# Performance work log

Measured on AMD Instinct MI355X. Metric: run time of the kernel, lower is better.

## Reference

```python
import jax, jax.numpy as jnp
from jax import lax
import numpy as np


def setup_inputs() -> dict:
    key = jax.random.key(0)
    k1, k2, k3 = jax.random.split(key, 3)
    B, H, W, C = 8, 128, 128, 128
    F, KS = 128, 3
    x = jax.random.normal(k1, (B, H, W, C), dtype=jnp.float32)
    style = jax.random.normal(k2, (B, C), dtype=jnp.float32)
    kernel = jax.random.normal(k3, (KS, KS, C, F), dtype=jnp.float32) * 0.05
    return {"x": x, "style": style, "kernel": kernel}


def reference(x, style, kernel):
    """StyleGAN2 modulated+demodulated conv via grouped conv (groups=batch).
    x: (B,H,W,C) NHWC, style: (B,C), kernel: (kh,kw,C,F)."""
    B, H, W, C = x.shape
    kh, kw, Cin, F = kernel.shape
    # Modulate: per-sample scale of input channels -> (B, kh, kw, C, F)
    w = kernel[None] * (style[:, None, None, :, None] + 1.0)
    # Demodulate: normalize each output filter over (kh, kw, Cin)
    w = w / jnp.sqrt(jnp.sum(jnp.square(w), axis=(1, 2, 3), keepdims=True) + 1e-8)
    # Grouped conv trick: fold batch into channels, groups = B
    xg = jnp.transpose(x, (0, 3, 1, 2)).reshape(1, B * C, H, W)   # (1, B*C, H, W)
    wg = jnp.transpose(w, (1, 2, 3, 0, 4)).reshape(kh, kw, Cin, B * F)  # HWIO
    y = lax.conv_general_dilated(
        xg, wg, window_strides=(1, 1), padding="SAME",
        dimension_numbers=("NCHW", "HWIO", "NCHW"),
        feature_group_count=B,
    )  # (1, B*F, H, W)
    y = y.reshape(B, F, H, W)
    return jnp.transpose(y, (0, 2, 3, 1))  # NHWC
```

## Files before the change

kernel.cpp:

```cpp
#include <hip/hip_runtime.h>

typedef __attribute__((ext_vector_type(8))) short short8;
typedef __attribute__((ext_vector_type(8))) unsigned short ushort8;
typedef __attribute__((ext_vector_type(4))) float f32x4;

static __device__ __forceinline__ unsigned short f2bf(float f) {
    union { float f; unsigned int u; } a; a.f = f;
    unsigned int u = a.u;
    return (unsigned short)((u + 0x7fffu + ((u >> 16) & 1u)) >> 16);
}

static __device__ __forceinline__ void gll16(const unsigned short* g, unsigned short* l) {
    __builtin_amdgcn_global_load_lds(
        (const __attribute__((address_space(1))) unsigned int*)g,
        (__attribute__((address_space(3))) unsigned int*)l, 16, 0, 0);
}

__global__ void prep_sumsq(const float* __restrict__ kern,
                           const float* __restrict__ style,
                           float* __restrict__ partial) {
    const int rs = blockIdx.x;
    const int b  = blockIdx.y;
    const int t  = threadIdx.x;
    __shared__ float sty[128];
    __shared__ float red[256];
    if (t < 128) sty[t] = style[b * 128 + t] + 1.0f;
    __syncthreads();
    const int f = t & 127, half = t >> 7;
    const float* kp = kern + (size_t)rs * 16384 + f;
    float s = 0.0f;
    #pragma unroll 8
    for (int c = half * 64; c < half * 64 + 64; ++c) {
        float w = kp[(size_t)c * 128] * sty[c];
        s += w * w;
    }
    red[t] = s;
    __syncthreads();
    if (t < 128) partial[((size_t)b * 9 + rs) * 128 + t] = red[t] + red[t + 128];
}

__global__ void prep_wt(const float* __restrict__ kern,
                        const float* __restrict__ style,
                        const float* __restrict__ partial,
                        unsigned short* __restrict__ wt) {
    const int rs = blockIdx.x, b = blockIdx.y;
    const int t  = threadIdx.x;
    __shared__ float sty[128], dm[128];
    __shared__ float ts[32][132];
    if (t < 128) {
        sty[t] = style[b * 128 + t] + 1.0f;
    } else {
        const int f = t - 128;
        float s = 0.0f;
        #pragma unroll
        for (int r = 0; r < 9; ++r) s += partial[((size_t)b * 9 + r) * 128 + f];
        dm[f] = rsqrtf(s + 1e-8f);
    }
    __syncthreads();
    const float* kp = kern + (size_t)rs * 16384;
    unsigned short* wp = wt + ((size_t)b * 9 + rs) * 16384;
    for (int c0 = 0; c0 < 128; c0 += 32) {
        {
            const int fi = (t & 31) * 4;
            const int ci = t >> 5;
            #pragma unroll
            for (int k = 0; k < 4; ++k) {
                const float4 v = *(const float4*)(kp + (size_t)(c0 + ci + 8 * k) * 128 + fi);
                ts[ci + 8 * k][fi + 0] = v.x;
                ts[ci + 8 * k][fi + 1] = v.y;
                ts[ci + 8 * k][fi + 2] = v.z;
                ts[ci + 8 * k][fi + 3] = v.w;
            }
        }
        __syncthreads();
        {
            const int cb = (t & 7) * 4;
            const int f2 = t >> 3;
            #pragma unroll
            for (int k = 0; k < 4; ++k) {
                const int f = f2 + 32 * k;
                ushort4 o;
                o.x = f2bf(ts[cb + 0][f] * sty[c0 + cb + 0] * dm[f]);
                o.y = f2bf(ts[cb + 1][f] * sty[c0 + cb + 1] * dm[f]);
                o.z = f2bf(ts[cb + 2][f] * sty[c0 + cb + 2] * dm[f]);
                o.w = f2bf(ts[cb + 3][f] * sty[c0 + cb + 3] * dm[f]);
                *(ushort4*)(wp + (size_t)f * 128 + c0 + cb) = o;
            }
        }
        __syncthreads();
    }
}

#define PROW 16640
#define PPLANE 2163200
__global__ void cvt_x(const float* __restrict__ x, unsigned short* __restrict__ xbf) {
    const int id = blockIdx.x * 256 + threadIdx.x;
    if (id >= 8 * 130 * 130 * 16) return;
    const int cg = id & 15;
    const int p  = id >> 4;
    const int wp = p % 130;
    const int q  = p / 130;
    const int hp = q % 130;
    const int b  = q / 130;
    ushort8 v = {0, 0, 0, 0, 0, 0, 0, 0};
    if (hp >= 1 && hp <= 128 && wp >= 1 && wp <= 128) {
        const float4* src = (const float4*)(x + (((size_t)b * 128 + (hp - 1)) * 128 + (wp - 1)) * 128 + cg * 8);
        float4 f0 = src[0];
        float4 f1 = src[1];
        v[0] = f2bf(f0.x); v[1] = f2bf(f0.y); v[2] = f2bf(f0.z); v[3] = f2bf(f0.w);
        v[4] = f2bf(f1.x); v[5] = f2bf(f1.y); v[6] = f2bf(f1.z); v[7] = f2bf(f1.w);
    }
    *(ushort8*)(xbf + (size_t)p * 128 + cg * 8) = v;
}

__global__ __launch_bounds__(256, 4) void mdconv6(const unsigned short* __restrict__ xbf,
                                                  const unsigned short* __restrict__ wt,
                                                  float* __restrict__ out) {
    const int lin = blockIdx.x;
    const int b   = lin & 7;
    const int h   = lin >> 3;
    const int tid = threadIdx.x;

    __shared__ unsigned short lsh[2 * 8192];

    const unsigned short* xb  = xbf + (size_t)b * PPLANE;
    const unsigned short* wtb = wt + (size_t)b * 9 * 16384;

    const int a0off = (tid >> 2) * 128 + (tid & 3) * 8;

    const int lane = tid & 63;
    const int wv   = tid >> 6;
    const int fl   = lane & 15;
    const int quad = lane >> 4;
    const int wrb  = (wv >> 1) * 64;
    const int fcb  = (wv & 1) * 64;
    const int ab_rd = (wrb + fl) * 32 + quad * 8;
    const int bb_rd = 4096 + (fcb + fl) * 32 + quad * 8;

    f32x4 acc[4][4];
    #pragma unroll
    for (int mt = 0; mt < 4; ++mt)
        #pragma unroll
        for (int ft = 0; ft < 4; ++ft)
            acc[mt][ft] = (f32x4){0.f, 0.f, 0.f, 0.f};

#define STAGE(st, nxt) {                                                          \
    const int rs_ = (st) >> 2, kc_ = (st) & 3;                                    \
    const int r_ = rs_ / 3, s_ = rs_ % 3;                                         \
    const unsigned short* ga = xb + ((size_t)(h + r_) * 130 + s_) * 128 + kc_ * 32; \
    const unsigned short* gb = wtb + rs_ * 16384 + kc_ * 32;                      \
    unsigned short* la = lsh + (nxt) * 8192;                                      \
    gll16(ga + a0off,        la + tid * 8);                                       \
    gll16(ga + a0off + 8192, la + 2048 + tid * 8);                                \
    gll16(gb + a0off,        la + 4096 + tid * 8);                                \
    gll16(gb + a0off + 8192, la + 6144 + tid * 8);                                \
}

    STAGE(0, 0);
    __syncthreads();

    #pragma unroll
    for (int st = 0; st < 36; ++st) {
        const int cur = st & 1;
        if (st < 35) STAGE(st + 1, cur ^ 1);
        const int ce = cur * 8192;
        short8 bv[4];
        #pragma unroll
        for (int ft = 0; ft < 4; ++ft)
            bv[ft] = *(const short8*)(lsh + ce + bb_rd + ft * 512);
        #pragma unroll
        for (int mt = 0; mt < 4; ++mt) {
            const short8 av = *(const short8*)(lsh + ce + ab_rd + mt * 512);
            #pragma unroll
            for (int ft = 0; ft < 4; ++ft)
                acc[mt][ft] = __builtin_amdgcn_mfma_f32_16x16x32_bf16(av, bv[ft], acc[mt][ft], 0, 0, 0);
        }
        __syncthreads();
    }
#undef STAGE

    float* ob = out + ((size_t)(b * 128 + h) * 128) * 128;
    #pragma unroll
    for (int mt = 0; mt < 4; ++mt) {
        #pragma unroll
        for (int reg = 0; reg < 4; ++reg) {
            const int w = wrb + mt * 16 + quad * 4 + reg;
            #pragma unroll
            for (int ft = 0; ft < 4; ++ft)
                ob[(size_t)w * 128 + fcb + ft * 16 + fl] = acc[mt][ft][reg];
        }
    }
}

__global__ void mdconv_fb(const float* __restrict__ x,
                          const unsigned short* __restrict__ wt,
                          float* __restrict__ out) {
    const int lin = blockIdx.x;
    const int b   = lin & 7;
    const int sp  = lin >> 3;
    const int h0  = (sp >> 3) * 8;
    const int w0  = (sp & 7) * 16;
    const int tid = threadIdx.x;
    __shared__ unsigned short xs[180 * 138];
    {
        const float* xb = x + (size_t)b * (128 * 128 * 128);
        for (int id = tid; id < 180 * 16; id += 256) {
            int p  = id >> 4;
            int cg = id & 15;
            int pr = p / 18;
            int pc = p - pr * 18;
            int hh = h0 - 1 + pr;
            int ww = w0 - 1 + pc;
            ushort8 v = {0, 0, 0, 0, 0, 0, 0, 0};
            if ((unsigned)hh < 128u && (unsigned)ww < 128u) {
                const float4* src = (const float4*)(xb + ((size_t)(hh * 128 + ww) * 128 + cg * 8));
                float4 f0 = src[0];
                float4 f1 = src[1];
                v[0] = f2bf(f0.x); v[1] = f2bf(f0.y); v[2] = f2bf(f0.z); v[3] = f2bf(f0.w);
                v[4] = f2bf(f1.x); v[5] = f2bf(f1.y); v[6] = f2bf(f1.z); v[7] = f2bf(f1.w);
            }
            *(ushort8*)(xs + p * 138 + cg * 8) = v;
        }
    }
    __syncthreads();
    const int lane = tid & 63;
    const int wave = tid >> 6;
    const int fl   = lane & 15;
    const int quad = lane >> 4;
    const int kq   = quad * 8;
    f32x4 acc[8][2];
    #pragma unroll
    for (int mt = 0; mt < 8; ++mt)
        #pragma unroll
        for (int j = 0; j < 2; ++j)
            acc[mt][j] = (f32x4){0.f, 0.f, 0.f, 0.f};
    const unsigned short* wtb = wt + (size_t)b * (9 * 128 * 128) + (size_t)wave * 4096 + fl * 128 + kq;
    #pragma unroll
    for (int rs = 0; rs < 9; ++rs) {
        const int r = rs / 3, s = rs % 3;
        #pragma unroll
        for (int kc = 0; kc < 4; ++kc) {
            const int k0 = kc * 32 + kq;
            short8 a[8];
            #pragma unroll
            for (int mt = 0; mt < 8; ++mt)
                a[mt] = *(const short8*)(xs + ((mt + r) * 18 + fl + s) * 138 + k0);
            #pragma unroll
            for (int j = 0; j < 2; ++j) {
                short8 bf = *(const short8*)(wtb + rs * 16384 + j * 2048 + kc * 32);
                #pragma unroll
                for (int mt = 0; mt < 8; ++mt)
                    acc[mt][j] = __builtin_amdgcn_mfma_f32_16x16x32_bf16(a[mt], bf, acc[mt][j], 0, 0, 0);
            }
        }
    }
    float* ob = out + ((size_t)(b * 128 + h0) * 128 + w0) * 128;
    #pragma unroll
    for (int mt = 0; mt < 8; ++mt)
        #pragma unroll
        for (int j = 0; j < 2; ++j) {
            const int f = (wave * 2 + j) * 16 + fl;
            #pragma unroll
            for (int reg = 0; reg < 4; ++reg)
                ob[((size_t)(mt * 128 + quad * 4 + reg)) * 128 + f] = acc[mt][j][reg];
        }
}

extern "C" void kernel_launch(void* const* d_in, const int* in_sizes, int n_in,
                              void* d_out, int out_size, void* d_ws, size_t ws_size,
                              hipStream_t stream) {
    const float* x     = (const float*)d_in[0];
    const float* style = (const float*)d_in[1];
    const float* kern  = (const float*)d_in[2];
    float* out = (float*)d_out;

    const size_t XBF_BYTES = (size_t)8 * 130 * 130 * 128 * 2;
    const size_t WT_BYTES  = (size_t)8 * 9 * 128 * 128 * 2;
    const size_t NEED      = XBF_BYTES + WT_BYTES + 36864;

    if (ws_size >= NEED) {
        unsigned short* xbf = (unsigned short*)d_ws;
        unsigned short* wt  = (unsigned short*)((char*)d_ws + XBF_BYTES);
        float* partial      = (float*)((char*)d_ws + XBF_BYTES + WT_BYTES);
        prep_sumsq<<<dim3(9, 8), dim3(256), 0, stream>>>(kern, style, partial);
        prep_wt<<<dim3(9, 8), dim3(256), 0, stream>>>(kern, style, partial, wt);
        cvt_x<<<dim3((8 * 130 * 130 * 16 + 255) / 256), dim3(256), 0, stream>>>(x, xbf);
        mdconv6<<<dim3(1024), dim3(256), 0, stream>>>(xbf, wt, out);
    } else {
        unsigned short* wt = (unsigned short*)d_ws;
        float* partial     = (float*)((char*)d_ws + WT_BYTES);
        prep_sumsq<<<dim3(9, 8), dim3(256), 0, stream>>>(kern, style, partial);
        prep_wt<<<dim3(9, 8), dim3(256), 0, stream>>>(kern, style, partial, wt);
        mdconv_fb<<<dim3(1024), dim3(256), 0, stream>>>(x, wt, out);
    }
}
```

Measured before the change: 165.6 us.

## Compute two output rows per block sharing weights; fuse sumsq and input conversion

The main conv kernel now runs 512-thread blocks that each compute two adjacent output rows, so every staged weight tile in LDS serves both rows, and the LDS layout is reorganised to match. This halves the global weight traffic per output row and halves the number of blocks. Separately, the sum-of-squares prep and the x-to-bf16 padded conversion are merged into one launch, removing a kernel launch. The cost is a larger LDS footprint per block and fewer, bigger blocks, which may lower occupancy.

```diff
diff --git a/kernel.cpp b/kernel.cpp
--- a/kernel.cpp
+++ b/kernel.cpp
@@ -16,27 +16,52 @@
         (__attribute__((address_space(3))) unsigned int*)l, 16, 0, 0);
 }
 
-__global__ void prep_sumsq(const float* __restrict__ kern,
-                           const float* __restrict__ style,
-                           float* __restrict__ partial) {
-    const int rs = blockIdx.x;
-    const int b  = blockIdx.y;
-    const int t  = threadIdx.x;
-    __shared__ float sty[128];
-    __shared__ float red[256];
-    if (t < 128) sty[t] = style[b * 128 + t] + 1.0f;
-    __syncthreads();
-    const int f = t & 127, half = t >> 7;
-    const float* kp = kern + (size_t)rs * 16384 + f;
-    float s = 0.0f;
-    #pragma unroll 8
-    for (int c = half * 64; c < half * 64 + 64; ++c) {
-        float w = kp[(size_t)c * 128] * sty[c];
-        s += w * w;
-    }
-    red[t] = s;
-    __syncthreads();
-    if (t < 128) partial[((size_t)b * 9 + rs) * 128 + t] = red[t] + red[t + 128];
+#define PROW 16640
+#define PPLANE 2163200
+
+__global__ void prep1(const float* __restrict__ x,
+                      const float* __restrict__ kern,
+                      const float* __restrict__ style,
+                      float* __restrict__ partial,
+                      unsigned short* __restrict__ xbf) {
+    const int t = threadIdx.x;
+    if (blockIdx.x < 72) {
+        const int rs = blockIdx.x % 9;
+        const int b  = blockIdx.x / 9;
+        __shared__ float sty[128];
+        __shared__ float red[256];
+        if (t < 128) sty[t] = style[b * 128 + t] + 1.0f;
+        __syncthreads();
+        const int f = t & 127, half = t >> 7;
+        const float* kp = kern + (size_t)rs * 16384 + f;
+        float s = 0.0f;
+        #pragma unroll 8
+        for (int c = half * 64; c < half * 64 + 64; ++c) {
+            float w = kp[(size_t)c * 128] * sty[c];
+            s += w * w;
+        }
+        red[t] = s;
+        __syncthreads();
+        if (t < 128) partial[((size_t)b * 9 + rs) * 128 + t] = red[t] + red[t + 128];
+    } else {
+        const int id = (blockIdx.x - 72) * 256 + t;
+        if (id >= 8 * 130 * 130 * 16) return;
+        const int cg = id & 15;
+        const int p  = id >> 4;
+        const int wp = p % 130;
+        const int q  = p / 130;
+        const int hp = q % 130;
+        const int b  = q / 130;
+        ushort8 v = {0, 0, 0, 0, 0, 0, 0, 0};
+        if (hp >= 1 && hp <= 128 && wp >= 1 && wp <= 128) {
+            const float4* src = (const float4*)(x + (((size_t)b * 128 + (hp - 1)) * 128 + (wp - 1)) * 128 + cg * 8);
+            float4 f0 = src[0];
+            float4 f1 = src[1];
+            v[0] = f2bf(f0.x); v[1] = f2bf(f0.y); v[2] = f2bf(f0.z); v[3] = f2bf(f0.w);
+            v[4] = f2bf(f1.x); v[5] = f2bf(f1.y); v[6] = f2bf(f1.z); v[7] = f2bf(f1.w);
+        }
+        *(ushort8*)(xbf + (size_t)p * 128 + cg * 8) = v;
+    }
 }
 
 __global__ void prep_wt(const float* __restrict__ kern,
@@ -91,51 +116,31 @@
     }
 }
 
-#define PROW 16640
-#define PPLANE 2163200
-__global__ void cvt_x(const float* __restrict__ x, unsigned short* __restrict__ xbf) {
-    const int id = blockIdx.x * 256 + threadIdx.x;
-    if (id >= 8 * 130 * 130 * 16) return;
-    const int cg = id & 15;
-    const int p  = id >> 4;
-    const int wp = p % 130;
-    const int q  = p / 130;
-    const int hp = q % 130;
-    const int b  = q / 130;
-    ushort8 v = {0, 0, 0, 0, 0, 0, 0, 0};
-    if (hp >= 1 && hp <= 128 && wp >= 1 && wp <= 128) {
-        const float4* src = (const float4*)(x + (((size_t)b * 128 + (hp - 1)) * 128 + (wp - 1)) * 128 + cg * 8);
-        float4 f0 = src[0];
-        float4 f1 = src[1];
-        v[0] = f2bf(f0.x); v[1] = f2bf(f0.y); v[2] = f2bf(f0.z); v[3] = f2bf(f0.w);
-        v[4] = f2bf(f1.x); v[5] = f2bf(f1.y); v[6] = f2bf(f1.z); v[7] = f2bf(f1.w);
-    }
-    *(ushort8*)(xbf + (size_t)p * 128 + cg * 8) = v;
-}
-
-__global__ __launch_bounds__(256, 4) void mdconv6(const unsigned short* __restrict__ xbf,
+__global__ __launch_bounds__(512, 4) void mdconv7(const unsigned short* __restrict__ xbf,
                                                   const unsigned short* __restrict__ wt,
                                                   float* __restrict__ out) {
     const int lin = blockIdx.x;
     const int b   = lin & 7;
-    const int h   = lin >> 3;
+    const int h2  = (lin >> 3) * 2;
     const int tid = threadIdx.x;
 
-    __shared__ unsigned short lsh[2 * 8192];
+    __shared__ unsigned short lsh[2 * 12288];
 
     const unsigned short* xb  = xbf + (size_t)b * PPLANE;
     const unsigned short* wtb = wt + (size_t)b * 9 * 16384;
 
-    const int a0off = (tid >> 2) * 128 + (tid & 3) * 8;
+    const int so = (tid & 127) * 128 + (tid >> 7) * 8;
 
     const int lane = tid & 63;
     const int wv   = tid >> 6;
+    const int hw   = wv >> 2;
+    const int ww   = (wv >> 1) & 1;
+    const int fw   = wv & 1;
     const int fl   = lane & 15;
     const int quad = lane >> 4;
-    const int wrb  = (wv >> 1) * 64;
-    const int fcb  = (wv & 1) * 64;
-    const int ab_rd = (wrb + fl) * 32 + quad * 8;
-    const int bb_rd = 4096 + (fcb + fl) * 32 + quad * 8;
+
+    const int ard = hw * 4096 + quad * 1024 + (ww * 64 + fl) * 8;
+    const int brd = 8192 + quad * 1024 + (fw * 64 + fl) * 8;
 
     f32x4 acc[4][4];
     #pragma unroll
@@ -147,13 +152,12 @@
 #define STAGE(st, nxt) {                                                          \
     const int rs_ = (st) >> 2, kc_ = (st) & 3;                                    \
     const int r_ = rs_ / 3, s_ = rs_ % 3;                                         \
-    const unsigned short* ga = xb + ((size_t)(h + r_) * 130 + s_) * 128 + kc_ * 32; \
-    const unsigned short* gb = wtb + rs_ * 16384 + kc_ * 32;                      \
-    unsigned short* la = lsh + (nxt) * 8192;                                      \
-    gll16(ga + a0off,        la + tid * 8);                                       \
-    gll16(ga + a0off + 8192, la + 2048 + tid * 8);                                \
-    gll16(gb + a0off,        la + 4096 + tid * 8);                                \
-    gll16(gb + a0off + 8192, la + 6144 + tid * 8);                                \
+    const unsigned short* ga0 = xb + ((size_t)(h2 + r_) * 130 + s_) * 128 + kc_ * 32; \
+    const unsigned short* gb  = wtb + rs_ * 16384 + kc_ * 32;                     \
+    unsigned short* la = lsh + (nxt) * 12288;                                     \
+    gll16(ga0 + so,        la + tid * 8);                                         \
+    gll16(ga0 + PROW + so, la + 4096 + tid * 8);                                  \
+    gll16(gb + so,         la + 8192 + tid * 8);                                  \
 }
 
     STAGE(0, 0);
@@ -163,14 +167,14 @@
     for (int st = 0; st < 36; ++st) {
         const int cur = st & 1;
         if (st < 35) STAGE(st + 1, cur ^ 1);
-        const int ce = cur * 8192;
+        const int ce = cur * 12288;
         short8 bv[4];
         #pragma unroll
         for (int ft = 0; ft < 4; ++ft)
-            bv[ft] = *(const short8*)(lsh + ce + bb_rd + ft * 512);
+            bv[ft] = *(const short8*)(lsh + ce + brd + ft * 128);
         #pragma unroll
         for (int mt = 0; mt < 4; ++mt) {
-            const short8 av = *(const short8*)(lsh + ce + ab_rd + mt * 512);
+            const short8 av = *(const short8*)(lsh + ce + ard + mt * 128);
             #pragma unroll
             for (int ft = 0; ft < 4; ++ft)
                 acc[mt][ft] = __builtin_amdgcn_mfma_f32_16x16x32_bf16(av, bv[ft], acc[mt][ft], 0, 0, 0);
@@ -179,17 +183,40 @@
     }
 #undef STAGE
 
-    float* ob = out + ((size_t)(b * 128 + h) * 128) * 128;
+    float* ob = out + ((size_t)(b * 128 + h2 + hw) * 128) * 128;
     #pragma unroll
     for (int mt = 0; mt < 4; ++mt) {
         #pragma unroll
         for (int reg = 0; reg < 4; ++reg) {
-            const int w = wrb + mt * 16 + quad * 4 + reg;
+            const int w = ww * 64 + mt * 16 + quad * 4 + reg;
             #pragma unroll
             for (int ft = 0; ft < 4; ++ft)
-                ob[(size_t)w * 128 + fcb + ft * 16 + fl] = acc[mt][ft][reg];
-        }
-    }
+                ob[(size_t)w * 128 + fw * 64 + ft * 16 + fl] = acc[mt][ft][reg];
+        }
+    }
+}
+
+__global__ void prep_sumsq(const float* __restrict__ kern,
+                           const float* __restrict__ style,
+                           float* __restrict__ partial) {
+    const int rs = blockIdx.x;
+    const int b  = blockIdx.y;
+    const int t  = threadIdx.x;
+    __shared__ float sty[128];
+    __shared__ float red[256];
+    if (t < 128) sty[t] = style[b * 128 + t] + 1.0f;
+    __syncthreads();
+    const int f = t & 127, half = t >> 7;
+    const float* kp = kern + (size_t)rs * 16384 + f;
+    float s = 0.0f;
+    #pragma unroll 8
+    for (int c = half * 64; c < half * 64 + 64; ++c) {
+        float w = kp[(size_t)c * 128] * sty[c];
+        s += w * w;
+    }
+    red[t] = s;
+    __syncthreads();
+    if (t < 128) partial[((size_t)b * 9 + rs) * 128 + t] = red[t] + red[t + 128];
 }
 
 __global__ void mdconv_fb(const float* __restrict__ x,
@@ -282,10 +309,9 @@
         unsigned short* xbf = (unsigned short*)d_ws;
         unsigned short* wt  = (unsigned short*)((char*)d_ws + XBF_BYTES);
         float* partial      = (float*)((char*)d_ws + XBF_BYTES + WT_BYTES);
-        prep_sumsq<<<dim3(9, 8), dim3(256), 0, stream>>>(kern, style, partial);
+        prep1<<<dim3(72 + 8450), dim3(256), 0, stream>>>(x, kern, style, partial, xbf);
         prep_wt<<<dim3(9, 8), dim3(256), 0, stream>>>(kern, style, partial, wt);
-        cvt_x<<<dim3((8 * 130 * 130 * 16 + 255) / 256), dim3(256), 0, stream>>>(x, xbf);
-        mdconv6<<<dim3(1024), dim3(256), 0, stream>>>(xbf, wt, out);
+        mdconv7<<<dim3(512), dim3(512), 0, stream>>>(xbf, wt, out);
     } else {
         unsigned short* wt = (unsigned short*)d_ws;
         float* partial     = (float*)((char*)d_ws + WT_BYTES);
```

Result: slower. 183.2 us (+10.7%).
